# Optimization experiments

Measured on AMD Instinct MI355X. Metric: run time of the kernel, lower is better.

Reference implementation:

```python
import jax, jax.numpy as jnp
import numpy as np

NQ = 4
PI_HALF = np.pi / 2
HAD = jnp.array([[1, 1], [1, -1]], dtype=jnp.complex64) / np.sqrt(2)
CNOT = jnp.array([[1, 0, 0, 0], [0, 1, 0, 0], [0, 0, 0, 1], [0, 0, 1, 0]], dtype=jnp.complex64)
_bits = (np.arange(2 ** NQ)[:, None] >> np.arange(NQ - 1, -1, -1)[None, :]) & 1
ZSIGNS = jnp.asarray(1.0 - 2.0 * _bits, jnp.float32)  # [16, NQ]


def _ry(theta):
    c = jnp.cos(theta / 2).astype(jnp.complex64)
    s = jnp.sin(theta / 2).astype(jnp.complex64)
    return jnp.stack([jnp.stack([c, -s], -1), jnp.stack([s, c], -1)], -2)  # [...,2,2]


def _rot(phi, theta, omega):
    # PennyLane Rot = RZ(omega) @ RY(theta) @ RZ(phi)
    c = jnp.cos(theta / 2).astype(jnp.complex64)
    s = jnp.sin(theta / 2).astype(jnp.complex64)
    ep = jnp.exp(0.5j * phi).astype(jnp.complex64)
    eo = jnp.exp(0.5j * omega).astype(jnp.complex64)
    return jnp.stack([jnp.stack([jnp.conj(ep) * jnp.conj(eo) * c, -ep * jnp.conj(eo) * s]),
                      jnp.stack([jnp.conj(ep) * eo * s, ep * eo * c])])


def _cry(theta):
    # controlled-RY, batched: [B] -> [B,4,4], basis order (control, target)
    B = theta.shape[0]
    U = jnp.zeros((B, 4, 4), jnp.complex64).at[:, 0, 0].set(1.0).at[:, 1, 1].set(1.0)
    return U.at[:, 2:, 2:].set(_ry(theta))


def _apply1(state, U, wire):
    s = jnp.moveaxis(state, wire + 1, 1)
    shp = s.shape
    s = s.reshape(shp[0], 2, -1)
    s = jnp.einsum('ij,bjk->bik', U, s) if U.ndim == 2 else jnp.einsum('bij,bjk->bik', U, s)
    return jnp.moveaxis(s.reshape(shp), 1, wire + 1)


def _apply2(state, U, q0, q1):
    s = jnp.moveaxis(state, (q0 + 1, q1 + 1), (1, 2))
    shp = s.shape
    s = s.reshape(shp[0], 4, -1)
    s = jnp.einsum('ij,bjk->bik', U, s) if U.ndim == 2 else jnp.einsum('bij,bjk->bik', U, s)
    return jnp.moveaxis(s.reshape(shp), (1, 2), (q0 + 1, q1 + 1))


def _init_state(B):
    s = jnp.zeros((B, 2 ** NQ), jnp.complex64).at[:, 0].set(1.0)
    return s.reshape((B,) + (2,) * NQ)


def _zexp(state):
    p = state.reshape(state.shape[0], -1)
    p = p.real ** 2 + p.imag ** 2
    return p @ ZSIGNS  # [B, NQ]


def _attention_circuit(q, k, params):
    # q, k: [E, NQ] angles; params: [NQ, 3] shared
    s = _init_state(q.shape[0])
    for i in range(NQ):
        s = _apply1(s, _ry(q[:, i]), i)
    for i in range(NQ):
        s = _apply1(s, HAD, i)
    for i in range(NQ):
        s = _apply2(s, _cry(k[:, i]), i, (i + 1) % NQ)
    for i in range(NQ):
        s = _apply1(s, _rot(params[i, 0], params[i, 1], params[i, 2]), i)
    return _zexp(s)


def _entangle_circuit(x, params):
    # x: [N, NQ] angles; params: [n_layers, NQ, 3]
    s = _init_state(x.shape[0])
    for i in range(NQ):
        s = _apply1(s, _ry(x[:, i]), i)
    for l in range(params.shape[0]):
        for i in range(NQ - 1):
            s = _apply2(s, CNOT, i, i + 1)
        for i in range(NQ):
            s = _apply1(s, _rot(params[l, i, 0], params[l, i, 1], params[l, i, 2]), i)
        s = _apply2(s, CNOT, 0, NQ - 1)  # n_qubits >= 4
    return _zexp(s)


def _path_circuit(x, params):
    # x: [N, NQ]; params: [3, NQ, 3]
    s = _init_state(x.shape[0])
    for i in range(NQ):
        s = _apply1(s, HAD, i)
    for i in range(NQ):
        s = _apply1(s, _ry(x[:, i]), i)
    for l in range(3):
        for i in range(NQ):
            s = _apply1(s, _rot(params[l, i, 0], params[l, i, 1], params[l, i, 2]), i)
        for i in range(NQ - 1):
            s = _apply2(s, CNOT, i, i + 1)
    return _zexp(s)


def _forward(x, W_in, b_in, lin_W, lin_b, qproj_W, qproj_b, ent_params,
             attq_W, attq_b, attk_W, attk_b, att_qp, path_params,
             path_in_W, path_in_b, path_out_W, path_out_b, out_W, out_b, edge_index):
    N = x.shape[0]
    loops = jnp.arange(N, dtype=edge_index.dtype)
    ei = jnp.concatenate([edge_index, jnp.stack([loops, loops])], axis=1)  # add_self_loops
    src, dst = ei[0], ei[1]
    h = jax.nn.relu(x @ W_in.T + b_in)
    for l in range(lin_W.shape[0]):
        x_cls = h @ lin_W[l].T + lin_b[l]
        xq = _entangle_circuit(jnp.tanh(h[:, :NQ]) * PI_HALF, ent_params[l])
        x_comb = x_cls + xq @ qproj_W[l].T + qproj_b[l]
        q = jnp.tanh(h @ attq_W[l].T + attq_b[l]) * PI_HALF
        k = jnp.tanh(h @ attk_W[l].T + attk_b[l]) * PI_HALF
        scores = _attention_circuit(q[src], k[dst], att_qp[l]).mean(axis=1)  # [E]
        att = jax.nn.softmax(scores)  # global softmax over all edges (faithful)
        h = jax.ops.segment_sum(att[:, None] * x_comb[src], dst, num_segments=N)
        h = jax.nn.relu(h)  # dropout is identity at eval
    pq = jnp.tanh(h @ path_in_W.T + path_in_b) * PI_HALF
    h = _path_circuit(pq, path_params) @ path_out_W.T + path_out_b
    return h @ out_W.T + out_b


def setup_inputs() -> dict:
    key = jax.random.key(0)
    ks = jax.random.split(key, 22)
    N, E, D_in, D_h, D_out, L = 20000, 300000, 64, 128, 32, 2
    w = lambda k, shape: jax.random.normal(k, shape, jnp.float32) * 0.1
    return {
        'x': jax.random.normal(ks[0], (N, D_in), jnp.float32),
        'W_in': w(ks[1], (D_h, D_in)), 'b_in': w(ks[2], (D_h,)),
        'lin_W': w(ks[3], (L, D_h, D_h)), 'lin_b': w(ks[4], (L, D_h)),
        'qproj_W': w(ks[5], (L, D_h, NQ)), 'qproj_b': w(ks[6], (L, D_h)),
        'ent_params': w(ks[7], (L, 2, NQ, 3)),
        'attq_W': w(ks[8], (L, NQ, D_h)), 'attq_b': w(ks[9], (L, NQ)),
        'attk_W': w(ks[10], (L, NQ, D_h)), 'attk_b': w(ks[11], (L, NQ)),
        'att_qp': w(ks[12], (L, NQ, 3)),
        'path_params': w(ks[13], (3, NQ, 3)),
        'path_in_W': w(ks[14], (NQ, D_h)), 'path_in_b': w(ks[15], (NQ,)),
        'path_out_W': w(ks[16], (D_h, NQ)), 'path_out_b': w(ks[17], (D_h,)),
        'out_W': w(ks[18], (D_out, D_h)), 'out_b': w(ks[19], (D_out,)),
        'edge_index': jax.random.randint(ks[20], (2, E), 0, N, dtype=jnp.int32),
    }


def reference(x, W_in, b_in, lin_W, lin_b, qproj_W, qproj_b, ent_params,
              attq_W, attq_b, attk_W, attk_b, att_qp, path_params,
              path_in_W, path_in_b, path_out_W, path_out_b, out_W, out_b, edge_index):
    return _forward(x, W_in, b_in, lin_W, lin_b, qproj_W, qproj_b, ent_params,
                    attq_W, attq_b, attk_W, attk_b, att_qp, path_params,
                    path_in_W, path_in_b, path_out_W, path_out_b, out_W, out_b, edge_index)
```

## Files before the change

kernel.cpp:

```cpp
#include <hip/hip_runtime.h>
#include <math.h>

#define PI_HALF 1.57079632679489662f

__device__ __forceinline__ float fast_tanh(float x) {
    float e = __expf(2.f * x);
    return 1.f - 2.f * __builtin_amdgcn_rcpf(e + 1.f);
}


__device__ __forceinline__ void init_state(float sr[16], float si[16]) {
#pragma unroll
    for (int i = 0; i < 16; ++i) { sr[i] = 0.f; si[i] = 0.f; }
    sr[0] = 1.f;
}

template<int M>
__device__ __forceinline__ void ry_g(float sr[16], float si[16], float c, float s) {
#pragma unroll
    for (int i = 0; i < 16; ++i) {
        if (i & M) continue;
        const int j = i | M;
        float ar = sr[i], ai = si[i], br = sr[j], bi = si[j];
        sr[i] = c * ar - s * br;  si[i] = c * ai - s * bi;
        sr[j] = s * ar + c * br;  si[j] = s * ai + c * bi;
    }
}

template<int M>
__device__ __forceinline__ void had_g(float sr[16], float si[16]) {
    const float r = 0.70710678118654752f;
#pragma unroll
    for (int i = 0; i < 16; ++i) {
        if (i & M) continue;
        const int j = i | M;
        float ar = sr[i], ai = si[i], br = sr[j], bi = si[j];
        sr[i] = (ar + br) * r;  si[i] = (ai + bi) * r;
        sr[j] = (ar - br) * r;  si[j] = (ai - bi) * r;
    }
}

template<int MC, int MT>
__device__ __forceinline__ void cnot_g(float sr[16], float si[16]) {
#pragma unroll
    for (int i = 0; i < 16; ++i) {
        if (!(i & MC) || (i & MT)) continue;
        const int j = i | MT;
        float tr = sr[i], ti = si[i];
        sr[i] = sr[j]; si[i] = si[j];
        sr[j] = tr;    si[j] = ti;
    }
}

template<int MC, int MT>
__device__ __forceinline__ void cry_g(float sr[16], float si[16], float c, float s) {
#pragma unroll
    for (int i = 0; i < 16; ++i) {
        if (!(i & MC) || (i & MT)) continue;
        const int j = i | MT;
        float ar = sr[i], ai = si[i], br = sr[j], bi = si[j];
        sr[i] = c * ar - s * br;  si[i] = c * ai - s * bi;
        sr[j] = s * ar + c * br;  si[j] = s * ai + c * bi;
    }
}

template<int M>
__device__ __forceinline__ void rot_pre(float sr[16], float si[16], const float* __restrict__ u) {
    const float u00r = u[0], u00i = u[1], u01r = u[2], u01i = u[3];
    const float u10r = u[4], u10i = u[5], u11r = u[6], u11i = u[7];
#pragma unroll
    for (int i = 0; i < 16; ++i) {
        if (i & M) continue;
        const int j = i | M;
        float ar = sr[i], ai = si[i], br = sr[j], bi = si[j];
        sr[i] = u00r * ar - u00i * ai + u01r * br - u01i * bi;
        si[i] = u00r * ai + u00i * ar + u01r * bi + u01i * br;
        sr[j] = u10r * ar - u10i * ai + u11r * br - u11i * bi;
        si[j] = u10r * ai + u10i * ar + u11r * bi + u11i * br;
    }
}

__device__ __forceinline__ void zexp_g(const float sr[16], const float si[16], float z[4]) {
    float p[16];
#pragma unroll
    for (int i = 0; i < 16; ++i) p[i] = sr[i] * sr[i] + si[i] * si[i];
    z[0] = z[1] = z[2] = z[3] = 0.f;
#pragma unroll
    for (int i = 0; i < 16; ++i) {
        z[0] += (i & 8) ? -p[i] : p[i];
        z[1] += (i & 4) ? -p[i] : p[i];
        z[2] += (i & 2) ? -p[i] : p[i];
        z[3] += (i & 1) ? -p[i] : p[i];
    }
}

__global__ void k_setup(const float* __restrict__ entp, const float* __restrict__ attqp,
                        const float* __restrict__ pparm,
                        const float* __restrict__ outW, const float* __restrict__ outb,
                        const float* __restrict__ poW, const float* __restrict__ pob,
                        float* __restrict__ rotbuf, float* __restrict__ M,
                        float* __restrict__ v) {
    const int t = threadIdx.x;
    if (t < 36) {
        const float* p;
        if (t < 16)      p = entp  + t * 3;
        else if (t < 24) p = attqp + (t - 16) * 3;
        else             p = pparm + (t - 24) * 3;
        float phi = p[0], theta = p[1], omega = p[2];
        float st, ct; sincosf(0.5f * theta, &st, &ct);
        float sp, cp; sincosf(0.5f * (phi + omega), &sp, &cp);
        float sm, cm; sincosf(0.5f * (phi - omega), &sm, &cm);
        float* u = rotbuf + t * 8;
        u[0] =  ct * cp;  u[1] = -ct * sp;
        u[2] = -st * cm;  u[3] = -st * sm;
        u[4] =  st * cm;  u[5] = -st * sm;
        u[6] =  ct * cp;  u[7] =  ct * sp;
    } else if (t >= 64 && t < 192) {
        int t2 = t - 64;
        int o = t2 >> 2, i = t2 & 3;
        float acc = 0.f;
        for (int j = 0; j < 128; ++j) acc += outW[o * 128 + j] * poW[j * 4 + i];
        M[t2] = acc;
    } else if (t >= 192 && t < 224) {
        int o = t - 192;
        float acc = outb[o];
        for (int j = 0; j < 128; ++j) acc += outW[o * 128 + j] * pob[j];
        v[o] = acc;
    }
}


__global__ void k_in(const float* __restrict__ x, const float* __restrict__ W,
                     const float* __restrict__ b, float* __restrict__ h, int N) {
    __shared__ float xs[16 * 64];
    const int base = blockIdx.x * 16;
    const int tid = threadIdx.x;
    for (int idx = tid; idx < 16 * 64; idx += 128) {
        int n = base + (idx >> 6);
        xs[idx] = (n < N) ? x[(size_t)n * 64 + (idx & 63)] : 0.f;
    }
    __syncthreads();
    float acc[16];
#pragma unroll
    for (int n = 0; n < 16; ++n) acc[n] = 0.f;
    const float4* wr4 = (const float4*)(W + tid * 64);
    for (int c4 = 0; c4 < 16; ++c4) {
        float4 w = wr4[c4];
#pragma unroll
        for (int n = 0; n < 16; ++n) {
            float4 hv = *(const float4*)&xs[n * 64 + c4 * 4];
            acc[n] += w.x * hv.x + w.y * hv.y + w.z * hv.z + w.w * hv.w;
        }
    }
    const float bb = b[tid];
#pragma unroll
    for (int n = 0; n < 16; ++n) {
        int node = base + n;
        if (node < N) h[(size_t)node * 128 + tid] = fmaxf(acc[n] + bb, 0.f);
    }
}

__global__ void k_ent(const float* __restrict__ h, const float* __restrict__ rotE,
                      float* __restrict__ xq, int N) {
    int n = blockIdx.x * blockDim.x + threadIdx.x;
    if (n >= N) return;
    float4 hv = *(const float4*)&h[(size_t)n * 128];
    float sr[16], si[16];
    init_state(sr, si);
    { float s, c; __sincosf(fast_tanh(hv.x) * (0.5f * PI_HALF), &s, &c); ry_g<8>(sr, si, c, s); }
    { float s, c; __sincosf(fast_tanh(hv.y) * (0.5f * PI_HALF), &s, &c); ry_g<4>(sr, si, c, s); }
    { float s, c; __sincosf(fast_tanh(hv.z) * (0.5f * PI_HALF), &s, &c); ry_g<2>(sr, si, c, s); }
    { float s, c; __sincosf(fast_tanh(hv.w) * (0.5f * PI_HALF), &s, &c); ry_g<1>(sr, si, c, s); }
#pragma unroll
    for (int l = 0; l < 2; ++l) {
        cnot_g<8, 4>(sr, si); cnot_g<4, 2>(sr, si); cnot_g<2, 1>(sr, si);
        const float* P = rotE + l * 32;
        rot_pre<8>(sr, si, P);
        rot_pre<4>(sr, si, P + 8);
        rot_pre<2>(sr, si, P + 16);
        rot_pre<1>(sr, si, P + 24);
        cnot_g<8, 1>(sr, si);
    }
    float z[4]; zexp_g(sr, si, z);
    *(float4*)&xq[(size_t)n * 4] = make_float4(z[0], z[1], z[2], z[3]);
}

__global__ void k_lin(const float* __restrict__ h, const float* __restrict__ xq,
                      const float* __restrict__ linW, const float* __restrict__ linb,
                      const float* __restrict__ qpW, const float* __restrict__ qpb,
                      const float* __restrict__ aqW, const float* __restrict__ aqb,
                      const float* __restrict__ akW, const float* __restrict__ akb,
                      float* __restrict__ xcomb, float* __restrict__ qbuf,
                      float* __restrict__ kbuf, int N) {
    __shared__ float hs[16 * 128];
    __shared__ float xqs[16 * 4];
    const int base = blockIdx.x * 16;
    const int tid = threadIdx.x;
    for (int idx = tid; idx < 16 * 128; idx += 128) {
        int n = base + (idx >> 7);
        hs[idx] = (n < N) ? h[(size_t)n * 128 + (idx & 127)] : 0.f;
    }
    if (tid < 64) {
        int n = base + (tid >> 2);
        xqs[tid] = (n < N) ? xq[(size_t)n * 4 + (tid & 3)] : 0.f;
    }
    __syncthreads();
    float acc[16];
#pragma unroll
    for (int n = 0; n < 16; ++n) acc[n] = 0.f;
    const float4* wr4 = (const float4*)(linW + tid * 128);
    for (int c4 = 0; c4 < 32; ++c4) {
        float4 w = wr4[c4];
#pragma unroll
        for (int n = 0; n < 16; ++n) {
            float4 hv = *(const float4*)&hs[n * 128 + c4 * 4];
            acc[n] += w.x * hv.x + w.y * hv.y + w.z * hv.z + w.w * hv.w;
        }
    }
    const float bb = linb[tid] + qpb[tid];
    const float qw0 = qpW[tid * 4 + 0], qw1 = qpW[tid * 4 + 1];
    const float qw2 = qpW[tid * 4 + 2], qw3 = qpW[tid * 4 + 3];
#pragma unroll
    for (int n = 0; n < 16; ++n) {
        int node = base + n;
        if (node < N) {
            xcomb[(size_t)node * 128 + tid] = acc[n] + bb
                + qw0 * xqs[n * 4 + 0] + qw1 * xqs[n * 4 + 1]
                + qw2 * xqs[n * 4 + 2] + qw3 * xqs[n * 4 + 3];
        }
    }
    const int nl = tid >> 3;
    const int which = tid & 7;
    const int qi = which & 3;
    const float4* Wp4 = (const float4*)(((which < 4) ? aqW : akW) + qi * 128);
    float dot = (which < 4) ? aqb[qi] : akb[qi];
    for (int c4 = 0; c4 < 32; ++c4) {
        float4 w = Wp4[c4];
        float4 hv = *(const float4*)&hs[nl * 128 + c4 * 4];
        dot += w.x * hv.x + w.y * hv.y + w.z * hv.z + w.w * hv.w;
    }
    int node = base + nl;
    if (node < N) {
        float half = fast_tanh(dot) * (0.5f * PI_HALF);
        float s, c; __sincosf(half, &s, &c);
        float* dst = ((which < 4) ? qbuf : kbuf) + (size_t)node * 8 + qi * 2;
        dst[0] = c; dst[1] = s;
    }
}

__global__ void k_att(const float* __restrict__ qb, const float* __restrict__ kb,
                      const int* __restrict__ ei, const float* __restrict__ RA,
                      const int* __restrict__ inv, float* __restrict__ escore,
                      float* __restrict__ sumexp, int E, int EP) {
    __shared__ float red[256];
    int e = blockIdx.x * blockDim.x + threadIdx.x;
    float ex = 0.f;
    if (e < EP) {
        int s_, d_;
        if (e < E) { s_ = ei[e]; d_ = ei[E + e]; } else { s_ = d_ = e - E; }
        float4 qa = *(const float4*)&qb[(size_t)s_ * 8];
        float4 qc = *(const float4*)&qb[(size_t)s_ * 8 + 4];
        float4 ka = *(const float4*)&kb[(size_t)d_ * 8];
        float4 kc = *(const float4*)&kb[(size_t)d_ * 8 + 4];
        float sr[16], si[16];
        init_state(sr, si);
        ry_g<8>(sr, si, qa.x, qa.y);
        ry_g<4>(sr, si, qa.z, qa.w);
        ry_g<2>(sr, si, qc.x, qc.y);
        ry_g<1>(sr, si, qc.z, qc.w);
        had_g<8>(sr, si); had_g<4>(sr, si); had_g<2>(sr, si); had_g<1>(sr, si);
        cry_g<8, 4>(sr, si, ka.x, ka.y);
        cry_g<4, 2>(sr, si, ka.z, ka.w);
        cry_g<2, 1>(sr, si, kc.x, kc.y);
        cry_g<1, 8>(sr, si, kc.z, kc.w);
        rot_pre<8>(sr, si, RA);
        rot_pre<4>(sr, si, RA + 8);
        rot_pre<2>(sr, si, RA + 16);
        rot_pre<1>(sr, si, RA + 24);
        float z[4]; zexp_g(sr, si, z);
        float sc = 0.25f * (z[0] + z[1] + z[2] + z[3]);
        ex = __expf(sc);
        escore[inv[e]] = ex;
    }
    red[threadIdx.x] = ex;
    __syncthreads();
    for (int s = 128; s > 0; s >>= 1) {
        if ((int)threadIdx.x < s) red[threadIdx.x] += red[threadIdx.x + s];
        __syncthreads();
    }
    if (threadIdx.x == 0) atomicAdd(sumexp, red[0]);
}


__global__ void k_hist(const int* __restrict__ ei, int* __restrict__ cnt, int E, int EP) {
    int e = blockIdx.x * blockDim.x + threadIdx.x;
    if (e >= EP) return;
    int d_ = (e < E) ? ei[E + e] : e - E;
    atomicAdd(&cnt[d_], 1);
}

__global__ void k_scan(const int* __restrict__ cnt, int* __restrict__ off,
                       int* __restrict__ cur, int N) {
    __shared__ int tot[1024];
    const int t = threadIdx.x;
    const int chunk = (N + 1023) >> 10;
    const int s0 = t * chunk;
    const int s1 = min(s0 + chunk, N);
    int sum = 0;
    for (int i = s0; i < s1; ++i) sum += cnt[i];
    tot[t] = sum;
    __syncthreads();
    for (int d = 1; d < 1024; d <<= 1) {
        int v = (t >= d) ? tot[t - d] : 0;
        __syncthreads();
        tot[t] += v;
        __syncthreads();
    }
    int run = (t == 0) ? 0 : tot[t - 1];
    for (int i = s0; i < s1; ++i) {
        off[i] = run; cur[i] = run;
        run += cnt[i];
    }
}

__global__ void k_fill(const int* __restrict__ ei, int* __restrict__ cur,
                       int* __restrict__ srcs, int* __restrict__ inv, int E, int EP) {
    int e = blockIdx.x * blockDim.x + threadIdx.x;
    if (e >= EP) return;
    int s_, d_;
    if (e < E) { s_ = ei[e]; d_ = ei[E + e]; } else { s_ = d_ = e - E; }
    int pos = atomicAdd(&cur[d_], 1);
    srcs[pos] = s_;
    inv[e] = pos;
}

__global__ void k_gather(const float* __restrict__ xcomb, const int* __restrict__ srcs,
                         const float* __restrict__ escore, const int* __restrict__ off,
                         const int* __restrict__ cnt, const float* __restrict__ sumexp,
                         float* __restrict__ h) {
    __shared__ int sS[128];
    __shared__ float wS[128];
    const int b = blockIdx.x;
    const int tid = threadIdx.x;
    const int start = off[b];
    const int num = cnt[b];
    float acc = 0.f;
    for (int base = 0; base < num; base += 128) {
        int m = min(128, num - base);
        if (tid < m) {
            sS[tid] = srcs[start + base + tid];
            wS[tid] = escore[start + base + tid];
        }
        __syncthreads();
        for (int i = 0; i < m; ++i)
            acc += wS[i] * xcomb[(size_t)sS[i] * 128 + tid];
        __syncthreads();
    }
    const float invS = __builtin_amdgcn_rcpf(sumexp[0]);
    h[(size_t)b * 128 + tid] = fmaxf(acc * invS, 0.f);
}

#define PQ_STRIDE 132
__global__ void k_pq(const float* __restrict__ h, const float* __restrict__ piW,
                     const float* __restrict__ pib, float* __restrict__ pq8, int N) {
    __shared__ float hs[32 * PQ_STRIDE];
    const int base = blockIdx.x * 32;
    const int tid = threadIdx.x;
    for (int idx = tid; idx < 32 * 128; idx += 128) {
        int n = base + (idx >> 7);
        hs[(idx >> 7) * PQ_STRIDE + (idx & 127)] = (n < N) ? h[(size_t)n * 128 + (idx & 127)] : 0.f;
    }
    __syncthreads();
    const int nl = tid >> 2;
    const int i  = tid & 3;
    float dot = pib[i];
    const float4* w4 = (const float4*)(piW + i * 128);
    for (int c4 = 0; c4 < 32; ++c4) {
        float4 w = w4[c4];
        float4 hv = *(const float4*)&hs[nl * PQ_STRIDE + c4 * 4];
        dot += w.x * hv.x + w.y * hv.y + w.z * hv.z + w.w * hv.w;
    }
    int node = base + nl;
    if (node < N) {
        float half = fast_tanh(dot) * (0.5f * PI_HALF);
        float s, c; __sincosf(half, &s, &c);
        pq8[(size_t)node * 8 + i * 2]     = c;
        pq8[(size_t)node * 8 + i * 2 + 1] = s;
    }
}

__global__ void k_pathc(const float* __restrict__ pq8, const float* __restrict__ RP,
                        const float* __restrict__ M, const float* __restrict__ v,
                        float* __restrict__ out, int N) {
    __shared__ float zS[256 * 4];
    __shared__ float MS[128];
    __shared__ float vS[32];
    const int tid = threadIdx.x;
    if (tid < 128) MS[tid] = M[tid];
    else if (tid < 160) vS[tid - 128] = v[tid - 128];
    __syncthreads();
    const int base = blockIdx.x * 256;
    const int n = base + tid;
    if (n < N) {
        float4 pa = *(const float4*)&pq8[(size_t)n * 8];
        float4 pc = *(const float4*)&pq8[(size_t)n * 8 + 4];
        float sr[16], si[16];
        init_state(sr, si);
        had_g<8>(sr, si); had_g<4>(sr, si); had_g<2>(sr, si); had_g<1>(sr, si);
        ry_g<8>(sr, si, pa.x, pa.y);
        ry_g<4>(sr, si, pa.z, pa.w);
        ry_g<2>(sr, si, pc.x, pc.y);
        ry_g<1>(sr, si, pc.z, pc.w);
#pragma unroll
        for (int l = 0; l < 3; ++l) {
            const float* P = RP + l * 32;
            rot_pre<8>(sr, si, P);
            rot_pre<4>(sr, si, P + 8);
            rot_pre<2>(sr, si, P + 16);
            rot_pre<1>(sr, si, P + 24);
            cnot_g<8, 4>(sr, si); cnot_g<4, 2>(sr, si); cnot_g<2, 1>(sr, si);
        }
        float z[4]; zexp_g(sr, si, z);
        zS[tid * 4 + 0] = z[0]; zS[tid * 4 + 1] = z[1];
        zS[tid * 4 + 2] = z[2]; zS[tid * 4 + 3] = z[3];
    }
    __syncthreads();
#pragma unroll
    for (int k = 0; k < 32; ++k) {
        int flat = k * 256 + tid;
        int nl = flat >> 5;
        int o = flat & 31;
        int node = base + nl;
        if (node < N) {
            out[(size_t)node * 32 + o] = vS[o]
                + MS[o * 4 + 0] * zS[nl * 4 + 0] + MS[o * 4 + 1] * zS[nl * 4 + 1]
                + MS[o * 4 + 2] * zS[nl * 4 + 2] + MS[o * 4 + 3] * zS[nl * 4 + 3];
        }
    }
}


extern "C" void kernel_launch(void* const* d_in, const int* in_sizes, int n_in,
                              void* d_out, int out_size, void* d_ws, size_t ws_size,
                              hipStream_t stream) {
    const float* x     = (const float*)d_in[0];
    const float* W_in  = (const float*)d_in[1];
    const float* b_in  = (const float*)d_in[2];
    const float* linW  = (const float*)d_in[3];
    const float* linb  = (const float*)d_in[4];
    const float* qpW   = (const float*)d_in[5];
    const float* qpb   = (const float*)d_in[6];
    const float* entp  = (const float*)d_in[7];
    const float* aqW   = (const float*)d_in[8];
    const float* aqb   = (const float*)d_in[9];
    const float* akW   = (const float*)d_in[10];
    const float* akb   = (const float*)d_in[11];
    const float* attqp = (const float*)d_in[12];
    const float* pparm = (const float*)d_in[13];
    const float* piW   = (const float*)d_in[14];
    const float* pib   = (const float*)d_in[15];
    const float* poW   = (const float*)d_in[16];
    const float* pob   = (const float*)d_in[17];
    const float* outW  = (const float*)d_in[18];
    const float* outb  = (const float*)d_in[19];
    const int*   ei    = (const int*)d_in[20];

    const int N  = in_sizes[0] / 64;
    const int E  = in_sizes[20] / 2;
    const int EP = E + N;

    float* ws     = (float*)d_ws;
    float* h      = ws;
    float* xcomb  = h      + (size_t)N * 128;
    float* xq     = xcomb  + (size_t)N * 128;
    float* qbuf   = xq     + (size_t)N * 4;
    float* kbuf   = qbuf   + (size_t)N * 8;
    float* pq8    = kbuf   + (size_t)N * 8;
    float* escore = pq8    + (size_t)N * 8;
    float* rotbuf = escore + EP;
    float* Mm     = rotbuf + 36 * 8;
    float* vv     = Mm + 128;
    int*   cnt    = (int*)(vv + 32);
    float* sumexp = (float*)(cnt + N);
    int*   off    = (int*)(sumexp + 4);
    int*   cur    = off + N;
    int*   srcs   = cur + N;
    int*   inv    = srcs + EP;

    const float* rotE = rotbuf;
    const float* rotA = rotbuf + 128;
    const float* rotP = rotbuf + 192;

    const int nb16 = (N + 15) / 16;
    const int ebl  = (EP + 255) / 256;

    hipMemsetAsync(cnt, 0, (size_t)(N + 4) * sizeof(int), stream);
    k_hist<<<ebl, 256, 0, stream>>>(ei, cnt, E, EP);
    k_scan<<<1, 1024, 0, stream>>>(cnt, off, cur, N);
    k_fill<<<ebl, 256, 0, stream>>>(ei, cur, srcs, inv, E, EP);
    k_setup<<<1, 256, 0, stream>>>(entp, attqp, pparm, outW, outb, poW, pob,
                                   rotbuf, Mm, vv);
    k_in<<<nb16, 128, 0, stream>>>(x, W_in, b_in, h, N);

    for (int l = 0; l < 2; ++l) {
        k_ent<<<(N + 255) / 256, 256, 0, stream>>>(h, rotE + l * 64, xq, N);
        k_lin<<<nb16, 128, 0, stream>>>(h, xq,
            linW + (size_t)l * 128 * 128, linb + l * 128,
            qpW + (size_t)l * 128 * 4, qpb + l * 128,
            aqW + (size_t)l * 4 * 128, aqb + l * 4,
            akW + (size_t)l * 4 * 128, akb + l * 4,
            xcomb, qbuf, kbuf, N);
        k_att<<<ebl, 256, 0, stream>>>(qbuf, kbuf, ei, rotA + l * 32, inv,
                                       escore, sumexp + l, E, EP);
        k_gather<<<N, 128, 0, stream>>>(xcomb, srcs, escore, off, cnt, sumexp + l, h);
    }

    k_pq<<<(N + 31) / 32, 128, 0, stream>>>(h, piW, pib, pq8, N);
    k_pathc<<<(N + 255) / 256, 256, 0, stream>>>(pq8, rotP, Mm, vv, (float*)d_out, N);
}
```

Before: 397.2 us.

## Fuse setup/fill/input kernels, fold entangler into lin, simplify circuits

Merges edge fill, parameter setup and input projection into one launch, folds the entangling circuit into the linear kernel, and fuses path projection with the path circuit in one tail kernel. Quantum circuits start from an analytic product state with real-only amplitudes until the first complex rotation, and the attention score is computed directly from a closed form over selected probabilities. Block reduction uses wavefront shuffles instead of a shared-memory tree. This cuts launch count, intermediate global buffers and redundant arithmetic, at the cost of serialising the entangler in 16 threads per block and a small 64-thread tail block with large shared memory.

```diff
diff --git a/kernel.cpp b/kernel.cpp
--- a/kernel.cpp
+++ b/kernel.cpp
@@ -9,34 +9,50 @@
 }
 
 
-__device__ __forceinline__ void init_state(float sr[16], float si[16]) {
-#pragma unroll
-    for (int i = 0; i < 16; ++i) { sr[i] = 0.f; si[i] = 0.f; }
-    sr[0] = 1.f;
+__device__ __forceinline__ void prod_init(float sr[16],
+        float c0, float s0, float c1, float s1,
+        float c2, float s2, float c3, float s3) {
+    float p2[4];
+    p2[0] = c0 * c1; p2[1] = c0 * s1; p2[2] = s0 * c1; p2[3] = s0 * s1;
+    float p3[8];
+#pragma unroll
+    for (int j = 0; j < 4; ++j) { p3[2 * j] = p2[j] * c2; p3[2 * j + 1] = p2[j] * s2; }
+#pragma unroll
+    for (int j = 0; j < 8; ++j) { sr[2 * j] = p3[j] * c3; sr[2 * j + 1] = p3[j] * s3; }
 }
 
 template<int M>
-__device__ __forceinline__ void ry_g(float sr[16], float si[16], float c, float s) {
+__device__ __forceinline__ void had_r(float sr[16]) {
+    const float r = 0.70710678118654752f;
 #pragma unroll
     for (int i = 0; i < 16; ++i) {
         if (i & M) continue;
         const int j = i | M;
-        float ar = sr[i], ai = si[i], br = sr[j], bi = si[j];
-        sr[i] = c * ar - s * br;  si[i] = c * ai - s * bi;
-        sr[j] = s * ar + c * br;  si[j] = s * ai + c * bi;
-    }
-}
-
-template<int M>
-__device__ __forceinline__ void had_g(float sr[16], float si[16]) {
-    const float r = 0.70710678118654752f;
-#pragma unroll
-    for (int i = 0; i < 16; ++i) {
-        if (i & M) continue;
-        const int j = i | M;
-        float ar = sr[i], ai = si[i], br = sr[j], bi = si[j];
-        sr[i] = (ar + br) * r;  si[i] = (ai + bi) * r;
-        sr[j] = (ar - br) * r;  si[j] = (ai - bi) * r;
+        float ar = sr[i], br = sr[j];
+        sr[i] = (ar + br) * r;
+        sr[j] = (ar - br) * r;
+    }
+}
+
+template<int MC, int MT>
+__device__ __forceinline__ void cry_r(float sr[16], float c, float s) {
+#pragma unroll
+    for (int i = 0; i < 16; ++i) {
+        if (!(i & MC) || (i & MT)) continue;
+        const int j = i | MT;
+        float ar = sr[i], br = sr[j];
+        sr[i] = c * ar - s * br;
+        sr[j] = s * ar + c * br;
+    }
+}
+
+template<int MC, int MT>
+__device__ __forceinline__ void cnot_r(float sr[16]) {
+#pragma unroll
+    for (int i = 0; i < 16; ++i) {
+        if (!(i & MC) || (i & MT)) continue;
+        const int j = i | MT;
+        float t = sr[i]; sr[i] = sr[j]; sr[j] = t;
     }
 }
 
@@ -49,18 +65,6 @@
         float tr = sr[i], ti = si[i];
         sr[i] = sr[j]; si[i] = si[j];
         sr[j] = tr;    si[j] = ti;
-    }
-}
-
-template<int MC, int MT>
-__device__ __forceinline__ void cry_g(float sr[16], float si[16], float c, float s) {
-#pragma unroll
-    for (int i = 0; i < 16; ++i) {
-        if (!(i & MC) || (i & MT)) continue;
-        const int j = i | MT;
-        float ar = sr[i], ai = si[i], br = sr[j], bi = si[j];
-        sr[i] = c * ar - s * br;  si[i] = c * ai - s * bi;
-        sr[j] = s * ar + c * br;  si[j] = s * ai + c * bi;
     }
 }
 
@@ -80,6 +84,22 @@
     }
 }
 
+template<int M>
+__device__ __forceinline__ void rot_first(float sr[16], float si[16], const float* __restrict__ u) {
+    const float u00r = u[0], u00i = u[1], u01r = u[2], u01i = u[3];
+    const float u10r = u[4], u10i = u[5], u11r = u[6], u11i = u[7];
+#pragma unroll
+    for (int i = 0; i < 16; ++i) {
+        if (i & M) continue;
+        const int j = i | M;
+        float ar = sr[i], br = sr[j];
+        sr[i] = u00r * ar + u01r * br;
+        si[i] = u00i * ar + u01i * br;
+        sr[j] = u10r * ar + u11r * br;
+        si[j] = u10i * ar + u11i * br;
+    }
+}
+
 __device__ __forceinline__ void zexp_g(const float sr[16], const float si[16], float z[4]) {
     float p[16];
 #pragma unroll
@@ -94,104 +114,97 @@
     }
 }
 
-__global__ void k_setup(const float* __restrict__ entp, const float* __restrict__ attqp,
-                        const float* __restrict__ pparm,
-                        const float* __restrict__ outW, const float* __restrict__ outb,
-                        const float* __restrict__ poW, const float* __restrict__ pob,
-                        float* __restrict__ rotbuf, float* __restrict__ M,
-                        float* __restrict__ v) {
-    const int t = threadIdx.x;
-    if (t < 36) {
-        const float* p;
-        if (t < 16)      p = entp  + t * 3;
-        else if (t < 24) p = attqp + (t - 16) * 3;
-        else             p = pparm + (t - 24) * 3;
-        float phi = p[0], theta = p[1], omega = p[2];
-        float st, ct; sincosf(0.5f * theta, &st, &ct);
-        float sp, cp; sincosf(0.5f * (phi + omega), &sp, &cp);
-        float sm, cm; sincosf(0.5f * (phi - omega), &sm, &cm);
-        float* u = rotbuf + t * 8;
-        u[0] =  ct * cp;  u[1] = -ct * sp;
-        u[2] = -st * cm;  u[3] = -st * sm;
-        u[4] =  st * cm;  u[5] = -st * sm;
-        u[6] =  ct * cp;  u[7] =  ct * sp;
-    } else if (t >= 64 && t < 192) {
-        int t2 = t - 64;
-        int o = t2 >> 2, i = t2 & 3;
-        float acc = 0.f;
-        for (int j = 0; j < 128; ++j) acc += outW[o * 128 + j] * poW[j * 4 + i];
-        M[t2] = acc;
-    } else if (t >= 192 && t < 224) {
-        int o = t - 192;
-        float acc = outb[o];
-        for (int j = 0; j < 128; ++j) acc += outW[o * 128 + j] * pob[j];
-        v[o] = acc;
-    }
-}
-
-
-__global__ void k_in(const float* __restrict__ x, const float* __restrict__ W,
-                     const float* __restrict__ b, float* __restrict__ h, int N) {
-    __shared__ float xs[16 * 64];
-    const int base = blockIdx.x * 16;
+
+__global__ void k_fsi(const int* __restrict__ ei, int* __restrict__ cur,
+                      int* __restrict__ srcs, int* __restrict__ inv, int E, int EP,
+                      const float* __restrict__ entp, const float* __restrict__ attqp,
+                      const float* __restrict__ pparm,
+                      const float* __restrict__ outW, const float* __restrict__ outb,
+                      const float* __restrict__ poW, const float* __restrict__ pob,
+                      float* __restrict__ rotbuf, float* __restrict__ M,
+                      float* __restrict__ v,
+                      const float* __restrict__ x, const float* __restrict__ W,
+                      const float* __restrict__ b, float* __restrict__ h,
+                      int N, int eblocks) {
+    __shared__ float xs[32 * 64];
+    const int bb = blockIdx.x;
     const int tid = threadIdx.x;
-    for (int idx = tid; idx < 16 * 64; idx += 128) {
+    if (bb < eblocks) {
+        int e = bb * 256 + tid;
+        if (e < EP) {
+            int s_, d_;
+            if (e < E) { s_ = ei[e]; d_ = ei[E + e]; } else { s_ = d_ = e - E; }
+            int pos = atomicAdd(&cur[d_], 1);
+            srcs[pos] = s_;
+            inv[e] = pos;
+        }
+        return;
+    }
+    if (bb == eblocks) {
+        const int t = tid;
+        if (t < 36) {
+            const float* p;
+            if (t < 16)      p = entp  + t * 3;
+            else if (t < 24) p = attqp + (t - 16) * 3;
+            else             p = pparm + (t - 24) * 3;
+            float phi = p[0], theta = p[1], omega = p[2];
+            float st, ct; sincosf(0.5f * theta, &st, &ct);
+            float sp, cp; sincosf(0.5f * (phi + omega), &sp, &cp);
+            float sm, cm; sincosf(0.5f * (phi - omega), &sm, &cm);
+            float* u = rotbuf + t * 8;
+            u[0] =  ct * cp;  u[1] = -ct * sp;
+            u[2] = -st * cm;  u[3] = -st * sm;
+            u[4] =  st * cm;  u[5] = -st * sm;
+            u[6] =  ct * cp;  u[7] =  ct * sp;
+        } else if (t >= 64 && t < 192) {
+            int t2 = t - 64;
+            int o = t2 >> 2, i = t2 & 3;
+            float acc = 0.f;
+            for (int j = 0; j < 128; ++j) acc += outW[o * 128 + j] * poW[j * 4 + i];
+            M[t2] = acc;
+        } else if (t >= 192 && t < 224) {
+            int o = t - 192;
+            float acc = outb[o];
+            for (int j = 0; j < 128; ++j) acc += outW[o * 128 + j] * pob[j];
+            v[o] = acc;
+        }
+        return;
+    }
+    const int base = (bb - eblocks - 1) * 32;
+    for (int idx = tid; idx < 32 * 64; idx += 256) {
         int n = base + (idx >> 6);
         xs[idx] = (n < N) ? x[(size_t)n * 64 + (idx & 63)] : 0.f;
     }
     __syncthreads();
+    const int ch = tid & 127;
+    const int half = tid >> 7;
     float acc[16];
 #pragma unroll
     for (int n = 0; n < 16; ++n) acc[n] = 0.f;
-    const float4* wr4 = (const float4*)(W + tid * 64);
+    const float4* wr4 = (const float4*)(W + ch * 64);
     for (int c4 = 0; c4 < 16; ++c4) {
         float4 w = wr4[c4];
 #pragma unroll
         for (int n = 0; n < 16; ++n) {
-            float4 hv = *(const float4*)&xs[n * 64 + c4 * 4];
+            float4 hv = *(const float4*)&xs[(half * 16 + n) * 64 + c4 * 4];
             acc[n] += w.x * hv.x + w.y * hv.y + w.z * hv.z + w.w * hv.w;
         }
     }
-    const float bb = b[tid];
+    const float bbv = b[ch];
 #pragma unroll
     for (int n = 0; n < 16; ++n) {
-        int node = base + n;
-        if (node < N) h[(size_t)node * 128 + tid] = fmaxf(acc[n] + bb, 0.f);
-    }
-}
-
-__global__ void k_ent(const float* __restrict__ h, const float* __restrict__ rotE,
-                      float* __restrict__ xq, int N) {
-    int n = blockIdx.x * blockDim.x + threadIdx.x;
-    if (n >= N) return;
-    float4 hv = *(const float4*)&h[(size_t)n * 128];
-    float sr[16], si[16];
-    init_state(sr, si);
-    { float s, c; __sincosf(fast_tanh(hv.x) * (0.5f * PI_HALF), &s, &c); ry_g<8>(sr, si, c, s); }
-    { float s, c; __sincosf(fast_tanh(hv.y) * (0.5f * PI_HALF), &s, &c); ry_g<4>(sr, si, c, s); }
-    { float s, c; __sincosf(fast_tanh(hv.z) * (0.5f * PI_HALF), &s, &c); ry_g<2>(sr, si, c, s); }
-    { float s, c; __sincosf(fast_tanh(hv.w) * (0.5f * PI_HALF), &s, &c); ry_g<1>(sr, si, c, s); }
-#pragma unroll
-    for (int l = 0; l < 2; ++l) {
-        cnot_g<8, 4>(sr, si); cnot_g<4, 2>(sr, si); cnot_g<2, 1>(sr, si);
-        const float* P = rotE + l * 32;
-        rot_pre<8>(sr, si, P);
-        rot_pre<4>(sr, si, P + 8);
-        rot_pre<2>(sr, si, P + 16);
-        rot_pre<1>(sr, si, P + 24);
-        cnot_g<8, 1>(sr, si);
-    }
-    float z[4]; zexp_g(sr, si, z);
-    *(float4*)&xq[(size_t)n * 4] = make_float4(z[0], z[1], z[2], z[3]);
-}
-
-__global__ void k_lin(const float* __restrict__ h, const float* __restrict__ xq,
-                      const float* __restrict__ linW, const float* __restrict__ linb,
-                      const float* __restrict__ qpW, const float* __restrict__ qpb,
-                      const float* __restrict__ aqW, const float* __restrict__ aqb,
-                      const float* __restrict__ akW, const float* __restrict__ akb,
-                      float* __restrict__ xcomb, float* __restrict__ qbuf,
-                      float* __restrict__ kbuf, int N) {
+        int node = base + half * 16 + n;
+        if (node < N) h[(size_t)node * 128 + ch] = fmaxf(acc[n] + bbv, 0.f);
+    }
+}
+
+__global__ void k_entlin(const float* __restrict__ h, const float* __restrict__ rotE2,
+                         const float* __restrict__ linW, const float* __restrict__ linb,
+                         const float* __restrict__ qpW, const float* __restrict__ qpb,
+                         const float* __restrict__ aqW, const float* __restrict__ aqb,
+                         const float* __restrict__ akW, const float* __restrict__ akb,
+                         float* __restrict__ xcomb, float* __restrict__ qbuf,
+                         float* __restrict__ kbuf, int N) {
     __shared__ float hs[16 * 128];
     __shared__ float xqs[16 * 4];
     const int base = blockIdx.x * 16;
@@ -200,9 +213,32 @@
         int n = base + (idx >> 7);
         hs[idx] = (n < N) ? h[(size_t)n * 128 + (idx & 127)] : 0.f;
     }
-    if (tid < 64) {
-        int n = base + (tid >> 2);
-        xqs[tid] = (n < N) ? xq[(size_t)n * 4 + (tid & 3)] : 0.f;
+    __syncthreads();
+    if (tid < 16) {
+        float4 hv = *(const float4*)&hs[tid * 128];
+        float c0, s0, c1, s1, c2, s2, c3, s3;
+        { float a = fast_tanh(hv.x) * (0.5f * PI_HALF); __sincosf(a, &s0, &c0); }
+        { float a = fast_tanh(hv.y) * (0.5f * PI_HALF); __sincosf(a, &s1, &c1); }
+        { float a = fast_tanh(hv.z) * (0.5f * PI_HALF); __sincosf(a, &s2, &c2); }
+        { float a = fast_tanh(hv.w) * (0.5f * PI_HALF); __sincosf(a, &s3, &c3); }
+        float sr[16], si[16];
+        prod_init(sr, c0, s0, c1, s1, c2, s2, c3, s3);
+        cnot_r<8, 4>(sr); cnot_r<4, 2>(sr); cnot_r<2, 1>(sr);
+        rot_first<8>(sr, si, rotE2);
+        rot_pre<4>(sr, si, rotE2 + 8);
+        rot_pre<2>(sr, si, rotE2 + 16);
+        rot_pre<1>(sr, si, rotE2 + 24);
+        cnot_g<8, 1>(sr, si);
+        cnot_g<8, 4>(sr, si); cnot_g<4, 2>(sr, si); cnot_g<2, 1>(sr, si);
+        const float* P = rotE2 + 32;
+        rot_pre<8>(sr, si, P);
+        rot_pre<4>(sr, si, P + 8);
+        rot_pre<2>(sr, si, P + 16);
+        rot_pre<1>(sr, si, P + 24);
+        cnot_g<8, 1>(sr, si);
+        float z[4]; zexp_g(sr, si, z);
+        xqs[tid * 4 + 0] = z[0]; xqs[tid * 4 + 1] = z[1];
+        xqs[tid * 4 + 2] = z[2]; xqs[tid * 4 + 3] = z[3];
     }
     __syncthreads();
     float acc[16];
@@ -241,8 +277,8 @@
     }
     int node = base + nl;
     if (node < N) {
-        float half = fast_tanh(dot) * (0.5f * PI_HALF);
-        float s, c; __sincosf(half, &s, &c);
+        float halfang = fast_tanh(dot) * (0.5f * PI_HALF);
+        float s, c; __sincosf(halfang, &s, &c);
         float* dst = ((which < 4) ? qbuf : kbuf) + (size_t)node * 8 + qi * 2;
         dst[0] = c; dst[1] = s;
     }
@@ -252,7 +288,7 @@
                       const int* __restrict__ ei, const float* __restrict__ RA,
                       const int* __restrict__ inv, float* __restrict__ escore,
                       float* __restrict__ sumexp, int E, int EP) {
-    __shared__ float red[256];
+    __shared__ float red[4];
     int e = blockIdx.x * blockDim.x + threadIdx.x;
     float ex = 0.f;
     if (e < EP) {
@@ -263,32 +299,36 @@
         float4 ka = *(const float4*)&kb[(size_t)d_ * 8];
         float4 kc = *(const float4*)&kb[(size_t)d_ * 8 + 4];
         float sr[16], si[16];
-        init_state(sr, si);
-        ry_g<8>(sr, si, qa.x, qa.y);
-        ry_g<4>(sr, si, qa.z, qa.w);
-        ry_g<2>(sr, si, qc.x, qc.y);
-        ry_g<1>(sr, si, qc.z, qc.w);
-        had_g<8>(sr, si); had_g<4>(sr, si); had_g<2>(sr, si); had_g<1>(sr, si);
-        cry_g<8, 4>(sr, si, ka.x, ka.y);
-        cry_g<4, 2>(sr, si, ka.z, ka.w);
-        cry_g<2, 1>(sr, si, kc.x, kc.y);
-        cry_g<1, 8>(sr, si, kc.z, kc.w);
-        rot_pre<8>(sr, si, RA);
+        prod_init(sr, qa.x, qa.y, qa.z, qa.w, qc.x, qc.y, qc.z, qc.w);
+        had_r<8>(sr); had_r<4>(sr); had_r<2>(sr); had_r<1>(sr);
+        cry_r<8, 4>(sr, ka.x, ka.y);
+        cry_r<4, 2>(sr, ka.z, ka.w);
+        cry_r<2, 1>(sr, kc.x, kc.y);
+        cry_r<1, 8>(sr, kc.z, kc.w);
+        rot_first<8>(sr, si, RA);
         rot_pre<4>(sr, si, RA + 8);
         rot_pre<2>(sr, si, RA + 16);
         rot_pre<1>(sr, si, RA + 24);
-        float z[4]; zexp_g(sr, si, z);
-        float sc = 0.25f * (z[0] + z[1] + z[2] + z[3]);
+        float p0  = sr[0]  * sr[0]  + si[0]  * si[0];
+        float p1  = sr[1]  * sr[1]  + si[1]  * si[1];
+        float p2  = sr[2]  * sr[2]  + si[2]  * si[2];
+        float p4  = sr[4]  * sr[4]  + si[4]  * si[4];
+        float p8  = sr[8]  * sr[8]  + si[8]  * si[8];
+        float p7  = sr[7]  * sr[7]  + si[7]  * si[7];
+        float p11 = sr[11] * sr[11] + si[11] * si[11];
+        float p13 = sr[13] * sr[13] + si[13] * si[13];
+        float p14 = sr[14] * sr[14] + si[14] * si[14];
+        float p15 = sr[15] * sr[15] + si[15] * si[15];
+        float sc = (p0 - p15) + 0.5f * ((p1 + p2 + p4 + p8) - (p7 + p11 + p13 + p14));
         ex = __expf(sc);
         escore[inv[e]] = ex;
     }
-    red[threadIdx.x] = ex;
-    __syncthreads();
-    for (int s = 128; s > 0; s >>= 1) {
-        if ((int)threadIdx.x < s) red[threadIdx.x] += red[threadIdx.x + s];
-        __syncthreads();
-    }
-    if (threadIdx.x == 0) atomicAdd(sumexp, red[0]);
+    float wsum = ex;
+#pragma unroll
+    for (int d = 32; d; d >>= 1) wsum += __shfl_xor(wsum, d, 64);
+    if ((threadIdx.x & 63) == 0) red[threadIdx.x >> 6] = wsum;
+    __syncthreads();
+    if (threadIdx.x == 0) atomicAdd(sumexp, red[0] + red[1] + red[2] + red[3]);
 }
 
 
@@ -321,17 +361,6 @@
         off[i] = run; cur[i] = run;
         run += cnt[i];
     }
-}
-
-__global__ void k_fill(const int* __restrict__ ei, int* __restrict__ cur,
-                       int* __restrict__ srcs, int* __restrict__ inv, int E, int EP) {
-    int e = blockIdx.x * blockDim.x + threadIdx.x;
-    if (e >= EP) return;
-    int s_, d_;
-    if (e < E) { s_ = ei[e]; d_ = ei[E + e]; } else { s_ = d_ = e - E; }
-    int pos = atomicAdd(&cur[d_], 1);
-    srcs[pos] = s_;
-    inv[e] = pos;
 }
 
 __global__ void k_gather(const float* __restrict__ xcomb, const int* __restrict__ srcs,
@@ -360,59 +389,59 @@
     h[(size_t)b * 128 + tid] = fmaxf(acc * invS, 0.f);
 }
 
-#define PQ_STRIDE 132
-__global__ void k_pq(const float* __restrict__ h, const float* __restrict__ piW,
-                     const float* __restrict__ pib, float* __restrict__ pq8, int N) {
-    __shared__ float hs[32 * PQ_STRIDE];
-    const int base = blockIdx.x * 32;
-    const int tid = threadIdx.x;
-    for (int idx = tid; idx < 32 * 128; idx += 128) {
-        int n = base + (idx >> 7);
-        hs[(idx >> 7) * PQ_STRIDE + (idx & 127)] = (n < N) ? h[(size_t)n * 128 + (idx & 127)] : 0.f;
-    }
-    __syncthreads();
-    const int nl = tid >> 2;
-    const int i  = tid & 3;
-    float dot = pib[i];
-    const float4* w4 = (const float4*)(piW + i * 128);
-    for (int c4 = 0; c4 < 32; ++c4) {
-        float4 w = w4[c4];
-        float4 hv = *(const float4*)&hs[nl * PQ_STRIDE + c4 * 4];
-        dot += w.x * hv.x + w.y * hv.y + w.z * hv.z + w.w * hv.w;
-    }
-    int node = base + nl;
-    if (node < N) {
-        float half = fast_tanh(dot) * (0.5f * PI_HALF);
-        float s, c; __sincosf(half, &s, &c);
-        pq8[(size_t)node * 8 + i * 2]     = c;
-        pq8[(size_t)node * 8 + i * 2 + 1] = s;
-    }
-}
-
-__global__ void k_pathc(const float* __restrict__ pq8, const float* __restrict__ RP,
-                        const float* __restrict__ M, const float* __restrict__ v,
-                        float* __restrict__ out, int N) {
-    __shared__ float zS[256 * 4];
+__global__ void k_tail(const float* __restrict__ h, const float* __restrict__ piW,
+                       const float* __restrict__ pib, const float* __restrict__ RP,
+                       const float* __restrict__ M, const float* __restrict__ v,
+                       float* __restrict__ out, int N) {
+    __shared__ float hs[64 * 132];
+    __shared__ float pqS[64 * 8];
+    __shared__ float zS[64 * 4];
     __shared__ float MS[128];
     __shared__ float vS[32];
     const int tid = threadIdx.x;
-    if (tid < 128) MS[tid] = M[tid];
-    else if (tid < 160) vS[tid - 128] = v[tid - 128];
-    __syncthreads();
-    const int base = blockIdx.x * 256;
-    const int n = base + tid;
-    if (n < N) {
-        float4 pa = *(const float4*)&pq8[(size_t)n * 8];
-        float4 pc = *(const float4*)&pq8[(size_t)n * 8 + 4];
+    const int base = blockIdx.x * 64;
+    MS[tid] = M[tid]; MS[tid + 64] = M[tid + 64];
+    if (tid < 32) vS[tid] = v[tid];
+    for (int idx = tid; idx < 64 * 128; idx += 64) {
+        int n = base + (idx >> 7);
+        hs[(idx >> 7) * 132 + (idx & 127)] = (n < N) ? h[(size_t)n * 128 + (idx & 127)] : 0.f;
+    }
+    __syncthreads();
+    for (int rep = 0; rep < 4; ++rep) {
+        int vt = rep * 64 + tid;
+        int nl = vt >> 2, i = vt & 3;
+        float dot = pib[i];
+        const float4* w4 = (const float4*)(piW + i * 128);
+        for (int c4 = 0; c4 < 32; ++c4) {
+            float4 w = w4[c4];
+            float4 hv = *(const float4*)&hs[nl * 132 + c4 * 4];
+            dot += w.x * hv.x + w.y * hv.y + w.z * hv.z + w.w * hv.w;
+        }
+        float halfang = fast_tanh(dot) * (0.5f * PI_HALF);
+        float s, c; __sincosf(halfang, &s, &c);
+        pqS[nl * 8 + i * 2]     = c;
+        pqS[nl * 8 + i * 2 + 1] = s;
+    }
+    __syncthreads();
+    {
+        const float r = 0.70710678118654752f;
+        float c0 = pqS[tid * 8 + 0], s0 = pqS[tid * 8 + 1];
+        float c1 = pqS[tid * 8 + 2], s1 = pqS[tid * 8 + 3];
+        float c2 = pqS[tid * 8 + 4], s2 = pqS[tid * 8 + 5];
+        float c3 = pqS[tid * 8 + 6], s3 = pqS[tid * 8 + 7];
+        float u0 = r * (c0 - s0), w0 = r * (c0 + s0);
+        float u1 = r * (c1 - s1), w1 = r * (c1 + s1);
+        float u2 = r * (c2 - s2), w2 = r * (c2 + s2);
+        float u3 = r * (c3 - s3), w3 = r * (c3 + s3);
         float sr[16], si[16];
-        init_state(sr, si);
-        had_g<8>(sr, si); had_g<4>(sr, si); had_g<2>(sr, si); had_g<1>(sr, si);
-        ry_g<8>(sr, si, pa.x, pa.y);
-        ry_g<4>(sr, si, pa.z, pa.w);
-        ry_g<2>(sr, si, pc.x, pc.y);
-        ry_g<1>(sr, si, pc.z, pc.w);
-#pragma unroll
-        for (int l = 0; l < 3; ++l) {
+        prod_init(sr, u0, w0, u1, w1, u2, w2, u3, w3);
+        rot_first<8>(sr, si, RP);
+        rot_pre<4>(sr, si, RP + 8);
+        rot_pre<2>(sr, si, RP + 16);
+        rot_pre<1>(sr, si, RP + 24);
+        cnot_g<8, 4>(sr, si); cnot_g<4, 2>(sr, si); cnot_g<2, 1>(sr, si);
+#pragma unroll
+        for (int l = 1; l < 3; ++l) {
             const float* P = RP + l * 32;
             rot_pre<8>(sr, si, P);
             rot_pre<4>(sr, si, P + 8);
@@ -427,7 +456,7 @@
     __syncthreads();
 #pragma unroll
     for (int k = 0; k < 32; ++k) {
-        int flat = k * 256 + tid;
+        int flat = k * 64 + tid;
         int nl = flat >> 5;
         int o = flat & 31;
         int node = base + nl;
@@ -472,11 +501,9 @@
     float* ws     = (float*)d_ws;
     float* h      = ws;
     float* xcomb  = h      + (size_t)N * 128;
-    float* xq     = xcomb  + (size_t)N * 128;
-    float* qbuf   = xq     + (size_t)N * 4;
+    float* qbuf   = xcomb  + (size_t)N * 128;
     float* kbuf   = qbuf   + (size_t)N * 8;
-    float* pq8    = kbuf   + (size_t)N * 8;
-    float* escore = pq8    + (size_t)N * 8;
+    float* escore = kbuf   + (size_t)N * 8;
     float* rotbuf = escore + EP;
     float* Mm     = rotbuf + 36 * 8;
     float* vv     = Mm + 128;
@@ -492,19 +519,18 @@
     const float* rotP = rotbuf + 192;
 
     const int nb16 = (N + 15) / 16;
+    const int nb32 = (N + 31) / 32;
     const int ebl  = (EP + 255) / 256;
 
     hipMemsetAsync(cnt, 0, (size_t)(N + 4) * sizeof(int), stream);
     k_hist<<<ebl, 256, 0, stream>>>(ei, cnt, E, EP);
     k_scan<<<1, 1024, 0, stream>>>(cnt, off, cur, N);
-    k_fill<<<ebl, 256, 0, stream>>>(ei, cur, srcs, inv, E, EP);
-    k_setup<<<1, 256, 0, stream>>>(entp, attqp, pparm, outW, outb, poW, pob,
-                                   rotbuf, Mm, vv);
-    k_in<<<nb16, 128, 0, stream>>>(x, W_in, b_in, h, N);
+    k_fsi<<<ebl + 1 + nb32, 256, 0, stream>>>(ei, cur, srcs, inv, E, EP,
+                                              entp, attqp, pparm, outW, outb, poW, pob,
+                                              rotbuf, Mm, vv, x, W_in, b_in, h, N, ebl);
 
     for (int l = 0; l < 2; ++l) {
-        k_ent<<<(N + 255) / 256, 256, 0, stream>>>(h, rotE + l * 64, xq, N);
-        k_lin<<<nb16, 128, 0, stream>>>(h, xq,
+        k_entlin<<<nb16, 128, 0, stream>>>(h, rotE + l * 64,
             linW + (size_t)l * 128 * 128, linb + l * 128,
             qpW + (size_t)l * 128 * 4, qpb + l * 128,
             aqW + (size_t)l * 4 * 128, aqb + l * 4,
@@ -515,6 +541,5 @@
         k_gather<<<N, 128, 0, stream>>>(xcomb, srcs, escore, off, cnt, sumexp + l, h);
     }
 
-    k_pq<<<(N + 31) / 32, 128, 0, stream>>>(h, piW, pib, pq8, N);
-    k_pathc<<<(N + 255) / 256, 256, 0, stream>>>(pq8, rotP, Mm, vv, (float*)d_out, N);
-}
+    k_tail<<<(N + 63) / 64, 64, 0, stream>>>(h, piW, pib, rotP, Mm, vv, (float*)d_out, N);
+}
```

Result: slower. 415.8 us (+4.7%).
